# Kernel optimization log

Hardware: AMD Instinct MI355X
Metric: run time of the kernel (lower is better)

The kernel has to match this reference:

```python
import jax, jax.numpy as jnp
import numpy as np

DIM = 512
HEADS = 8
DIM_HEAD = 64
SCALE = DIM_HEAD ** -0.5


def setup_inputs() -> dict:
    key = jax.random.key(0)
    ks = jax.random.split(key, 4)
    b, n = 4, 2048
    x = jax.random.normal(ks[0], (b, n, DIM), dtype=jnp.float32)
    Wq = jax.random.normal(ks[1], (DIM, HEADS * DIM_HEAD), dtype=jnp.float32) * (DIM ** -0.5)
    Wkv = jax.random.normal(ks[2], (DIM, 2 * HEADS * DIM_HEAD), dtype=jnp.float32) * (DIM ** -0.5)
    Wo = jax.random.normal(ks[3], (HEADS * DIM_HEAD, DIM), dtype=jnp.float32) * ((HEADS * DIM_HEAD) ** -0.5)
    bo = jnp.zeros((DIM,), dtype=jnp.float32)
    return {"x": x, "Wq": Wq, "Wkv": Wkv, "Wo": Wo, "bo": bo}


def reference(x, Wq, Wkv, Wo, bo):
    b, n, _ = x.shape
    # context = x (self-attention path, kv_include_self=False)
    q = x @ Wq                      # [b, n, h*d]
    kv = x @ Wkv                    # [b, n, 2*h*d]
    k, v = jnp.split(kv, 2, axis=-1)

    def split_heads(t):
        return t.reshape(b, n, HEADS, DIM_HEAD).transpose(0, 2, 1, 3)  # [b,h,n,d]

    q, k, v = split_heads(q), split_heads(k), split_heads(v)
    dots = jnp.einsum('bhid,bhjd->bhij', q, k) * SCALE  # [b,h,n,n]
    attn = jax.nn.softmax(dots, axis=-1)
    out = jnp.einsum('bhij,bhjd->bhid', attn, v)        # [b,h,n,d]
    out = out.transpose(0, 2, 1, 3).reshape(b, n, HEADS * DIM_HEAD)
    return out @ Wo + bo
```

## Files before the change

kernel.cpp:

```cpp
#include <hip/hip_runtime.h>
#include <hip/hip_bf16.h>

typedef short bf16x8 __attribute__((ext_vector_type(8)));
typedef float fx4    __attribute__((ext_vector_type(4)));

#if __has_builtin(__builtin_amdgcn_exp2f)
#define EXP2 __builtin_amdgcn_exp2f
#else
#define EXP2 exp2f
#endif

__device__ __forceinline__ unsigned pk2(float a, float b) {
  union { __hip_bfloat162 h; unsigned u; } cv;
  cv.h = __float22bfloat162_rn(float2{a, b});
  return cv.u;
}
__device__ __forceinline__ uint2 pk4(const fx4& v) {
  uint2 r;
  r.x = pk2(v[0], v[1]);
  r.y = pk2(v[2], v[3]);
  return r;
}

__device__ __forceinline__ void gld16(const void* g, void* l) {
  __builtin_amdgcn_global_load_lds(
      (const __attribute__((address_space(1))) unsigned int*)g,
      (__attribute__((address_space(3))) unsigned int*)l, 16, 0, 0);
}

__device__ __forceinline__ void bar_raw() {
  asm volatile("s_barrier" ::: "memory");
}
__device__ __forceinline__ void bar_lgkm() {
  asm volatile("s_waitcnt lgkmcnt(0)\ns_barrier" ::: "memory");
}
__device__ __forceinline__ void bar_lgkm_vm4() {
  asm volatile("s_waitcnt vmcnt(4) lgkmcnt(0)\ns_barrier" ::: "memory");
}
__device__ __forceinline__ void cfence() { asm volatile("" ::: "memory"); }

__global__ __launch_bounds__(256) void prep_kernel(
    const float* __restrict__ x, const float* __restrict__ Wq,
    const float* __restrict__ Wkv, const float* __restrict__ Wo,
    short* __restrict__ xb, short* __restrict__ WallT, short* __restrict__ WoT,
    float qscale) {
  const int bx = blockIdx.x, tid = threadIdx.x;
  if (bx < 4096) {
    int i = bx * 256 + tid;
    const float4 s = *(const float4*)(x + (size_t)i * 4);
    uint2 o; o.x = pk2(s.x, s.y); o.y = pk2(s.z, s.w);
    *(uint2*)(xb + (size_t)i * 4) = o;
    return;
  }
  __shared__ float t[32][33];
  const int idx = bx - 4096;
  const int wb = idx & 63, kt = (idx >> 6) * 32;
  const bool mode0 = wb < 48;
  const int ct = (mode0 ? wb : wb - 48) * 32;
  const int tx = tid & 31, ty = tid >> 5;
  short* outT = mode0 ? WallT : WoT;
#pragma unroll
  for (int s = 0; s < 4; ++s) {
    int k = kt + ty + s * 8;
    int c = ct + tx;
    float v;
    if (mode0) v = (c < 512) ? Wq[(size_t)k * 512 + c] * qscale
                             : Wkv[(size_t)k * 1024 + (c - 512)];
    else       v = Wo[(size_t)k * 512 + c];
    t[ty + s * 8][tx] = v;
  }
  __syncthreads();
#pragma unroll
  for (int s = 0; s < 4; ++s) {
    int c = ct + ty + s * 8;
    int k = kt + tx;
    unsigned u = __float_as_uint(t[tx][ty + s * 8]);
    u = (u + 0x7fffu + ((u >> 16) & 1u)) >> 16;
    outT[(size_t)c * 512 + k] = (short)u;
  }
}

__global__ __launch_bounds__(256) void gemm_qkv(
    const short* __restrict__ A, const short* __restrict__ Bt,
    short* __restrict__ oq, short* __restrict__ ok, short* __restrict__ ovT) {
  __shared__ short As[2 * 128 * 32];
  __shared__ short Bs[2 * 128 * 32];
  const int K = 512;
  const int tid = threadIdx.x;
  const int wave = tid >> 6, lane = tid & 63;
  const int quad = lane >> 4, l15 = lane & 15;
  const int wm = wave >> 1, wn = wave & 1;
  const int m0 = blockIdx.y * 128, n0 = blockIdx.x * 128;
  const bool swapped = (n0 < 1024);

  int arow[4], aoff[4];
#pragma unroll
  for (int c = 0; c < 4; ++c) {
    int u = c * 256 + tid;
    int slab = u >> 9, r2 = u & 511;
    arow[c] = r2 >> 2;
    aoff[c] = slab * 32 + (r2 & 3) * 8;
  }

  fx4 acc[4][4];
#pragma unroll
  for (int i = 0; i < 4; ++i)
#pragma unroll
    for (int j = 0; j < 4; ++j) acc[i][j] = fx4{0.f, 0.f, 0.f, 0.f};

  bf16x8 apre[4];
#pragma unroll
  for (int c = 0; c < 4; ++c)
    apre[c] = *(const bf16x8*)(A + (size_t)(m0 + arow[c]) * K + aoff[c]);

  for (int k0 = 0; k0 < K; k0 += 64) {
    bar_raw();
#pragma unroll
    for (int c = 0; c < 4; ++c)
      *(bf16x8*)(As + (size_t)(c * 256 + tid) * 8) = apre[c];
#pragma unroll
    for (int c = 0; c < 4; ++c) {
      int u = c * 256 + tid;
      int slab = u >> 9, r2 = u & 511;
      gld16(Bt + (size_t)(n0 + (r2 >> 2)) * K + k0 + slab * 32 + (r2 & 3) * 8,
            Bs + (size_t)(c * 256 + wave * 64) * 8);
    }
    cfence();
    {
      int kn = (k0 + 64) & 511;
#pragma unroll
      for (int c = 0; c < 4; ++c)
        apre[c] = *(const bf16x8*)(A + (size_t)(m0 + arow[c]) * K + kn + aoff[c]);
    }
    bar_lgkm_vm4();

#pragma unroll
    for (int ks2 = 0; ks2 < 2; ++ks2) {
      bf16x8 af[4], bfr[4];
#pragma unroll
      for (int i = 0; i < 4; ++i)
        af[i] = *(const bf16x8*)(As + ks2 * 4096 + (wm * 64 + i * 16 + l15) * 32 + quad * 8);
#pragma unroll
      for (int i = 0; i < 4; ++i)
        bfr[i] = *(const bf16x8*)(Bs + ks2 * 4096 + (wn * 64 + i * 16 + l15) * 32 + quad * 8);
      if (swapped) {
#pragma unroll
        for (int mi = 0; mi < 4; ++mi)
#pragma unroll
          for (int ni = 0; ni < 4; ++ni)
            acc[mi][ni] = __builtin_amdgcn_mfma_f32_16x16x32_bf16(bfr[ni], af[mi], acc[mi][ni], 0, 0, 0);
      } else {
#pragma unroll
        for (int mi = 0; mi < 4; ++mi)
#pragma unroll
          for (int ni = 0; ni < 4; ++ni)
            acc[mi][ni] = __builtin_amdgcn_mfma_f32_16x16x32_bf16(af[mi], bfr[ni], acc[mi][ni], 0, 0, 0);
      }
    }
  }

  const int rowb = m0 + wm * 64;
  const int colb = n0 + wn * 64;
  const int cls = n0 >> 9;
  if (cls < 2) {
    short* base = (cls == 0) ? oq : ok;
#pragma unroll
    for (int mi = 0; mi < 4; ++mi) {
      int t = rowb + mi * 16 + l15;
      int bb = t >> 11, ii = t & 2047;
#pragma unroll
      for (int ni = 0; ni < 4; ++ni) {
        int f = (colb + ni * 16 + quad * 4) & 511;
        int hh = f >> 6, dd = f & 63;
        *(uint2*)(base + ((size_t)(bb * 8 + hh) * 2048 + ii) * 64 + dd) = pk4(acc[mi][ni]);
      }
    }
  } else {
#pragma unroll
    for (int mi = 0; mi < 4; ++mi) {
      int rbase = rowb + mi * 16 + quad * 4;
      int bb = rbase >> 11;
      int ii = rbase & 2047;
#pragma unroll
      for (int ni = 0; ni < 4; ++ni) {
        int c = (colb + ni * 16 + l15) & 511;
        int hh = c >> 6, dd = c & 63;
        *(uint2*)(ovT + ((size_t)(bb * 8 + hh) * 64 + dd) * 2048 + ii) = pk4(acc[mi][ni]);
      }
    }
  }
}

__global__ __launch_bounds__(256) void gemm_out(
    const short* __restrict__ A, const short* __restrict__ Bt,
    float* __restrict__ of, const float* __restrict__ bias) {
  __shared__ short As[2 * 64 * 32];
  __shared__ short Bs[2 * 128 * 32];
  const int K = 512, N = 512;
  const int tid = threadIdx.x;
  const int wave = tid >> 6, lane = tid & 63;
  const int quad = lane >> 4, l15 = lane & 15;
  const int wm = wave >> 1, wn = wave & 1;
  const int m0 = blockIdx.y * 64, n0 = blockIdx.x * 128;

  int arow[2], aoff[2], brow[4], boff[4];
#pragma unroll
  for (int c = 0; c < 2; ++c) {
    int u = c * 256 + tid;
    int slab = u >> 8, r2 = u & 255;
    arow[c] = r2 >> 2; aoff[c] = slab * 32 + (r2 & 3) * 8;
  }
#pragma unroll
  for (int c = 0; c < 4; ++c) {
    int u = c * 256 + tid;
    int slab = u >> 9, r2 = u & 511;
    brow[c] = r2 >> 2; boff[c] = slab * 32 + (r2 & 3) * 8;
  }

  fx4 acc[2][4];
#pragma unroll
  for (int i = 0; i < 2; ++i)
#pragma unroll
    for (int j = 0; j < 4; ++j) acc[i][j] = fx4{0.f, 0.f, 0.f, 0.f};

  bf16x8 apre[2], bpre[4];
#pragma unroll
  for (int c = 0; c < 2; ++c)
    apre[c] = *(const bf16x8*)(A + (size_t)(m0 + arow[c]) * K + aoff[c]);
#pragma unroll
  for (int c = 0; c < 4; ++c)
    bpre[c] = *(const bf16x8*)(Bt + (size_t)(n0 + brow[c]) * K + boff[c]);

  for (int k0 = 0; k0 < K; k0 += 64) {
    bar_raw();
#pragma unroll
    for (int c = 0; c < 2; ++c)
      *(bf16x8*)(As + (size_t)(c * 256 + tid) * 8) = apre[c];
#pragma unroll
    for (int c = 0; c < 4; ++c)
      *(bf16x8*)(Bs + (size_t)(c * 256 + tid) * 8) = bpre[c];
    {
      int kn = (k0 + 64) & 511;
#pragma unroll
      for (int c = 0; c < 2; ++c)
        apre[c] = *(const bf16x8*)(A + (size_t)(m0 + arow[c]) * K + kn + aoff[c]);
#pragma unroll
      for (int c = 0; c < 4; ++c)
        bpre[c] = *(const bf16x8*)(Bt + (size_t)(n0 + brow[c]) * K + kn + boff[c]);
    }
    bar_lgkm();

#pragma unroll
    for (int ks2 = 0; ks2 < 2; ++ks2) {
      bf16x8 af[2], bfr[4];
#pragma unroll
      for (int i = 0; i < 2; ++i)
        af[i] = *(const bf16x8*)(As + ks2 * 2048 + (wm * 32 + i * 16 + l15) * 32 + quad * 8);
#pragma unroll
      for (int i = 0; i < 4; ++i)
        bfr[i] = *(const bf16x8*)(Bs + ks2 * 4096 + (wn * 64 + i * 16 + l15) * 32 + quad * 8);
#pragma unroll
      for (int mi = 0; mi < 2; ++mi)
#pragma unroll
        for (int ni = 0; ni < 4; ++ni)
          acc[mi][ni] = __builtin_amdgcn_mfma_f32_16x16x32_bf16(af[mi], bfr[ni], acc[mi][ni], 0, 0, 0);
    }
  }

  const int rowb = m0 + wm * 32;
  const int colb = n0 + wn * 64;
#pragma unroll
  for (int mi = 0; mi < 2; ++mi)
#pragma unroll
    for (int ni = 0; ni < 4; ++ni) {
      int cg = colb + ni * 16 + l15;
      float bv = bias[cg];
#pragma unroll
      for (int r = 0; r < 4; ++r) {
        int rg = rowb + mi * 16 + quad * 4 + r;
        of[(size_t)rg * N + cg] = acc[mi][ni][r] + bv;
      }
    }
}

__global__ __launch_bounds__(256) void attn_kernel(
    const short* __restrict__ Q, const short* __restrict__ K,
    const short* __restrict__ Vt, short* __restrict__ O) {
  __shared__ short Ks[64 * 64];
  __shared__ short Vs[64 * 64];
  __shared__ short Ps[4 * 32 * 72];

  const int tid = threadIdx.x;
  const int wave = tid >> 6, lane = tid & 63;
  const int quad = lane >> 4, l15 = lane & 15;
  const int bh = blockIdx.y;
  const int b = bh >> 3, h = bh & 7;
  const int i0 = blockIdx.x * 128 + wave * 32;
  short* Pw = Ps + wave * (32 * 72);

  const int idx0 = tid, idx1 = 256 + tid;
  const int row0 = idx0 >> 3, sg0 = (idx0 & 7) ^ (row0 & 7);
  const int row1 = idx1 >> 3, sg1 = (idx1 & 7) ^ (row1 & 7);
  const short* Kb = K + (size_t)bh * 2048 * 64;
  const short* Vb = Vt + (size_t)bh * 64 * 2048;

  bf16x8 qf[2][2];
#pragma unroll
  for (int it = 0; it < 2; ++it)
#pragma unroll
    for (int ks = 0; ks < 2; ++ks)
      qf[it][ks] = *(const bf16x8*)(Q + ((size_t)bh * 2048 + i0 + it * 16 + l15) * 64 + ks * 32 + quad * 8);

  bf16x8 ones;
#pragma unroll
  for (int c = 0; c < 8; ++c) ones[c] = (short)0x3F80;

  fx4 oacc[2][4];
  fx4 acc_l[2] = { fx4{0.f,0.f,0.f,0.f}, fx4{0.f,0.f,0.f,0.f} };
#pragma unroll
  for (int it = 0; it < 2; ++it)
#pragma unroll
    for (int dt = 0; dt < 4; ++dt) oacc[it][dt] = fx4{0.f, 0.f, 0.f, 0.f};

  bf16x8 kpre0, kpre1, vpre0, vpre1;
  kpre0 = *(const bf16x8*)(Kb + (size_t)row0 * 64 + sg0 * 8);
  kpre1 = *(const bf16x8*)(Kb + (size_t)row1 * 64 + sg1 * 8);
  vpre0 = *(const bf16x8*)(Vb + (size_t)row0 * 2048 + sg0 * 8);
  vpre1 = *(const bf16x8*)(Vb + (size_t)row1 * 2048 + sg1 * 8);

  for (int j0 = 0; j0 < 2048; j0 += 64) {
    bar_raw();
    *(bf16x8*)(Ks + idx0 * 8) = kpre0;
    *(bf16x8*)(Ks + idx1 * 8) = kpre1;
    *(bf16x8*)(Vs + idx0 * 8) = vpre0;
    *(bf16x8*)(Vs + idx1 * 8) = vpre1;
    cfence();
    {
      int jn = (j0 + 64) & 2047;
      kpre0 = *(const bf16x8*)(Kb + (size_t)(jn + row0) * 64 + sg0 * 8);
      kpre1 = *(const bf16x8*)(Kb + (size_t)(jn + row1) * 64 + sg1 * 8);
      vpre0 = *(const bf16x8*)(Vb + (size_t)row0 * 2048 + jn + sg0 * 8);
      vpre1 = *(const bf16x8*)(Vb + (size_t)row1 * 2048 + jn + sg1 * 8);
    }
    bar_lgkm();

    fx4 s[2][4];
#pragma unroll
    for (int it = 0; it < 2; ++it)
#pragma unroll
      for (int jt = 0; jt < 4; ++jt) s[it][jt] = fx4{0.f, 0.f, 0.f, 0.f};
#pragma unroll
    for (int ks = 0; ks < 2; ++ks) {
#pragma unroll
      for (int jt = 0; jt < 4; ++jt) {
        bf16x8 kf = *(const bf16x8*)(Ks + (jt * 16 + l15) * 64 + (((ks * 4 + quad) ^ (l15 & 7)) * 8));
#pragma unroll
        for (int it = 0; it < 2; ++it)
          s[it][jt] = __builtin_amdgcn_mfma_f32_16x16x32_bf16(kf, qf[it][ks], s[it][jt], 0, 0, 0);
      }
    }

#pragma unroll
    for (int it = 0; it < 2; ++it)
#pragma unroll
      for (int jt = 0; jt < 4; ++jt) {
#pragma unroll
        for (int r = 0; r < 4; ++r) s[it][jt][r] = EXP2(s[it][jt][r]);
        *(uint2*)(Pw + (it * 16 + l15) * 72 + jt * 16 + quad * 4) = pk4(s[it][jt]);
      }

#pragma unroll
    for (int kj = 0; kj < 2; ++kj) {
      bf16x8 pf[2];
#pragma unroll
      for (int it = 0; it < 2; ++it) {
        pf[it] = *(const bf16x8*)(Pw + (it * 16 + l15) * 72 + kj * 32 + quad * 8);
        acc_l[it] = __builtin_amdgcn_mfma_f32_16x16x32_bf16(ones, pf[it], acc_l[it], 0, 0, 0);
      }
#pragma unroll
      for (int dt = 0; dt < 4; ++dt) {
        bf16x8 vf = *(const bf16x8*)(Vs + (dt * 16 + l15) * 64 + (((kj * 4 + quad) ^ (l15 & 7)) * 8));
#pragma unroll
        for (int it = 0; it < 2; ++it)
          oacc[it][dt] = __builtin_amdgcn_mfma_f32_16x16x32_bf16(vf, pf[it], oacc[it][dt], 0, 0, 0);
      }
    }
  }

#pragma unroll
  for (int it = 0; it < 2; ++it) {
    float inv = __builtin_amdgcn_rcpf(acc_l[it][0]);
    size_t rowbase = ((size_t)b * 2048 + i0 + it * 16 + l15) * 512 + h * 64;
#pragma unroll
    for (int dt = 0; dt < 4; ++dt) {
      fx4 o = oacc[it][dt] * inv;
      *(uint2*)(O + rowbase + dt * 16 + quad * 4) = pk4(o);
    }
  }
}

extern "C" void kernel_launch(void* const* d_in, const int* in_sizes, int n_in,
                              void* d_out, int out_size, void* d_ws, size_t ws_size,
                              hipStream_t stream) {
  const float* x   = (const float*)d_in[0];
  const float* Wq  = (const float*)d_in[1];
  const float* Wkv = (const float*)d_in[2];
  const float* Wo  = (const float*)d_in[3];
  const float* bo  = (const float*)d_in[4];
  float* out = (float*)d_out;

  char* p = (char*)d_ws;
  short* xb    = (short*)p; p += (size_t)8192 * 512 * 2;
  short* WallT = (short*)p; p += (size_t)1536 * 512 * 2;
  short* WoT   = (short*)p; p += (size_t)512 * 512 * 2;
  short* qb    = (short*)p; p += (size_t)32 * 2048 * 64 * 2;
  short* kb    = (short*)p; p += (size_t)32 * 2048 * 64 * 2;
  short* vTb   = (short*)p; p += (size_t)32 * 64 * 2048 * 2;
  short* Ob    = (short*)p; p += (size_t)8192 * 512 * 2;

  const float qscale = 0.125f * 1.4426950408889634f;

  prep_kernel<<<5120, 256, 0, stream>>>(x, Wq, Wkv, Wo, xb, WallT, WoT, qscale);
  gemm_qkv<<<dim3(12, 64), 256, 0, stream>>>(xb, WallT, qb, kb, vTb);
  attn_kernel<<<dim3(16, 32), 256, 0, stream>>>(qb, kb, vTb, Ob);
  gemm_out<<<dim3(4, 128), 256, 0, stream>>>(Ob, WoT, out, bo);
}
```

Before: 165.0 us.

## Double-buffer K/V via direct global-to-LDS loads and shuffle P in registers

The attention kernel now keeps two K/V tiles in LDS and fills the next one with global_load_lds while the current tile is computed. This replaces the register-staged prefetch that needed separate LDS stores and two barriers per iteration. The softmax probabilities P are also rearranged into MFMA operand layout using permlane32/16 swaps, so they no longer round-trip through an LDS scratch buffer. In exchange, each iteration waits on vmcnt(0) at one barrier, and the correctness of the lane permutation and of the LDS write layout of the direct loads is assumed to match the swizzle.

```diff
diff --git a/kernel.cpp b/kernel.cpp
--- a/kernel.cpp
+++ b/kernel.cpp
@@ -3,6 +3,7 @@
 
 typedef short bf16x8 __attribute__((ext_vector_type(8)));
 typedef float fx4    __attribute__((ext_vector_type(4)));
+typedef unsigned uint32x2 __attribute__((ext_vector_type(2)));
 
 #if __has_builtin(__builtin_amdgcn_exp2f)
 #define EXP2 __builtin_amdgcn_exp2f
@@ -36,6 +37,9 @@
 }
 __device__ __forceinline__ void bar_lgkm_vm4() {
   asm volatile("s_waitcnt vmcnt(4) lgkmcnt(0)\ns_barrier" ::: "memory");
+}
+__device__ __forceinline__ void bar_vm_lgkm() {
+  asm volatile("s_waitcnt vmcnt(0) lgkmcnt(0)\ns_barrier" ::: "memory");
 }
 __device__ __forceinline__ void cfence() { asm volatile("" ::: "memory"); }
 
@@ -286,9 +290,8 @@
 __global__ __launch_bounds__(256) void attn_kernel(
     const short* __restrict__ Q, const short* __restrict__ K,
     const short* __restrict__ Vt, short* __restrict__ O) {
-  __shared__ short Ks[64 * 64];
-  __shared__ short Vs[64 * 64];
-  __shared__ short Ps[4 * 32 * 72];
+  __shared__ short Ks[2 * 64 * 64];
+  __shared__ short Vs[2 * 64 * 64];
 
   const int tid = threadIdx.x;
   const int wave = tid >> 6, lane = tid & 63;
@@ -296,7 +299,6 @@
   const int bh = blockIdx.y;
   const int b = bh >> 3, h = bh & 7;
   const int i0 = blockIdx.x * 128 + wave * 32;
-  short* Pw = Ps + wave * (32 * 72);
 
   const int idx0 = tid, idx1 = 256 + tid;
   const int row0 = idx0 >> 3, sg0 = (idx0 & 7) ^ (row0 & 7);
@@ -322,27 +324,24 @@
 #pragma unroll
     for (int dt = 0; dt < 4; ++dt) oacc[it][dt] = fx4{0.f, 0.f, 0.f, 0.f};
 
-  bf16x8 kpre0, kpre1, vpre0, vpre1;
-  kpre0 = *(const bf16x8*)(Kb + (size_t)row0 * 64 + sg0 * 8);
-  kpre1 = *(const bf16x8*)(Kb + (size_t)row1 * 64 + sg1 * 8);
-  vpre0 = *(const bf16x8*)(Vb + (size_t)row0 * 2048 + sg0 * 8);
-  vpre1 = *(const bf16x8*)(Vb + (size_t)row1 * 2048 + sg1 * 8);
+  gld16(Kb + (size_t)row0 * 64 + sg0 * 8, Ks + wave * 512);
+  gld16(Kb + (size_t)row1 * 64 + sg1 * 8, Ks + 2048 + wave * 512);
+  gld16(Vb + (size_t)row0 * 2048 + sg0 * 8, Vs + wave * 512);
+  gld16(Vb + (size_t)row1 * 2048 + sg1 * 8, Vs + 2048 + wave * 512);
 
   for (int j0 = 0; j0 < 2048; j0 += 64) {
-    bar_raw();
-    *(bf16x8*)(Ks + idx0 * 8) = kpre0;
-    *(bf16x8*)(Ks + idx1 * 8) = kpre1;
-    *(bf16x8*)(Vs + idx0 * 8) = vpre0;
-    *(bf16x8*)(Vs + idx1 * 8) = vpre1;
-    cfence();
-    {
-      int jn = (j0 + 64) & 2047;
-      kpre0 = *(const bf16x8*)(Kb + (size_t)(jn + row0) * 64 + sg0 * 8);
-      kpre1 = *(const bf16x8*)(Kb + (size_t)(jn + row1) * 64 + sg1 * 8);
-      vpre0 = *(const bf16x8*)(Vb + (size_t)row0 * 2048 + jn + sg0 * 8);
-      vpre1 = *(const bf16x8*)(Vb + (size_t)row1 * 2048 + jn + sg1 * 8);
-    }
-    bar_lgkm();
+    const int cur = (j0 >> 6) & 1;
+    bar_vm_lgkm();
+    if (j0 + 64 < 2048) {
+      const int jn = j0 + 64;
+      const int nb = (cur ^ 1) * 4096;
+      gld16(Kb + (size_t)(jn + row0) * 64 + sg0 * 8, Ks + nb + wave * 512);
+      gld16(Kb + (size_t)(jn + row1) * 64 + sg1 * 8, Ks + nb + 2048 + wave * 512);
+      gld16(Vb + (size_t)row0 * 2048 + jn + sg0 * 8, Vs + nb + wave * 512);
+      gld16(Vb + (size_t)row1 * 2048 + jn + sg1 * 8, Vs + nb + 2048 + wave * 512);
+    }
+    const short* Kc = Ks + cur * 4096;
+    const short* Vc = Vs + cur * 4096;
 
     fx4 s[2][4];
 #pragma unroll
@@ -353,36 +352,49 @@
     for (int ks = 0; ks < 2; ++ks) {
 #pragma unroll
       for (int jt = 0; jt < 4; ++jt) {
-        bf16x8 kf = *(const bf16x8*)(Ks + (jt * 16 + l15) * 64 + (((ks * 4 + quad) ^ (l15 & 7)) * 8));
+        bf16x8 kf = *(const bf16x8*)(Kc + (jt * 16 + l15) * 64 + (((ks * 4 + quad) ^ (l15 & 7)) * 8));
 #pragma unroll
         for (int it = 0; it < 2; ++it)
           s[it][jt] = __builtin_amdgcn_mfma_f32_16x16x32_bf16(kf, qf[it][ks], s[it][jt], 0, 0, 0);
       }
     }
 
-#pragma unroll
-    for (int it = 0; it < 2; ++it)
+    bf16x8 pfr[2][2];
+#pragma unroll
+    for (int it = 0; it < 2; ++it) {
+      unsigned W[4][2];
 #pragma unroll
       for (int jt = 0; jt < 4; ++jt) {
 #pragma unroll
         for (int r = 0; r < 4; ++r) s[it][jt][r] = EXP2(s[it][jt][r]);
-        *(uint2*)(Pw + (it * 16 + l15) * 72 + jt * 16 + quad * 4) = pk4(s[it][jt]);
-      }
+        W[jt][0] = pk2(s[it][jt][0], s[it][jt][1]);
+        W[jt][1] = pk2(s[it][jt][2], s[it][jt][3]);
+      }
+#pragma unroll
+      for (int k = 0; k < 2; ++k) {
+        union { unsigned u[4]; bf16x8 v; } pw;
+#pragma unroll
+        for (int hh = 0; hh < 2; ++hh) {
+          uint32x2 a = __builtin_amdgcn_permlane32_swap(W[2 * k][hh], W[2 * k + 1][hh], false, false);
+          uint32x2 t = __builtin_amdgcn_permlane16_swap(a[0], a[1], false, false);
+          pw.u[hh] = t[0];
+          pw.u[2 + hh] = t[1];
+        }
+        pfr[it][k] = pw.v;
+      }
+    }
 
 #pragma unroll
     for (int kj = 0; kj < 2; ++kj) {
-      bf16x8 pf[2];
-#pragma unroll
-      for (int it = 0; it < 2; ++it) {
-        pf[it] = *(const bf16x8*)(Pw + (it * 16 + l15) * 72 + kj * 32 + quad * 8);
-        acc_l[it] = __builtin_amdgcn_mfma_f32_16x16x32_bf16(ones, pf[it], acc_l[it], 0, 0, 0);
-      }
+#pragma unroll
+      for (int it = 0; it < 2; ++it)
+        acc_l[it] = __builtin_amdgcn_mfma_f32_16x16x32_bf16(ones, pfr[it][kj], acc_l[it], 0, 0, 0);
 #pragma unroll
       for (int dt = 0; dt < 4; ++dt) {
-        bf16x8 vf = *(const bf16x8*)(Vs + (dt * 16 + l15) * 64 + (((kj * 4 + quad) ^ (l15 & 7)) * 8));
+        bf16x8 vf = *(const bf16x8*)(Vc + (dt * 16 + l15) * 64 + (((kj * 4 + quad) ^ (l15 & 7)) * 8));
 #pragma unroll
         for (int it = 0; it < 2; ++it)
-          oacc[it][dt] = __builtin_amdgcn_mfma_f32_16x16x32_bf16(vf, pf[it], oacc[it][dt], 0, 0, 0);
+          oacc[it][dt] = __builtin_amdgcn_mfma_f32_16x16x32_bf16(vf, pfr[it][kj], oacc[it][dt], 0, 0, 0);
       }
     }
   }
```

New measurement: 167.5 us. About the same (+1.5%).
